# Optimization experiments

Hardware: AMD Instinct MI355X
Metric: run time of the kernel (lower is better)

## Reference

```python
import jax, jax.numpy as jnp
import numpy as np

B = 128
K = 16
# (in_ch, featdim, dim) per stage, matching conv1..conv11
DIMS = [(3, 8, 2048), (8, 32, 1024), (32, 64, 512), (64, 64, 256), (64, 64, 128),
        (64, 128, 64), (128, 256, 32), (256, 512, 16), (512, 512, 8), (512, 512, 4),
        (512, 1024, 2)]


def setup_inputs() -> dict:
    key = jax.random.key(0)
    ks = jax.random.split(key, 64)
    inp = {"x": jax.random.normal(ks[0], (B, 3, 2048), dtype=jnp.float32)}
    i = 1
    for li, (cin, cf, d) in enumerate(DIMS, start=1):
        inp[f"W{li}"] = jax.random.normal(ks[i], (3 * cf, cin), dtype=jnp.float32) / np.sqrt(cin).astype(np.float32); i += 1
        inp[f"b{li}"] = jax.random.normal(ks[i], (3 * cf,), dtype=jnp.float32) * 0.01; i += 1
        inp[f"sel{li}"] = jax.random.randint(ks[i], (d,), 0, 3); i += 1
    inp["fcW"] = jax.random.normal(ks[i], (K, 1024), dtype=jnp.float32) / np.sqrt(1024).astype(np.float32); i += 1
    inp["fcb"] = jax.random.normal(ks[i], (K,), dtype=jnp.float32) * 0.01
    return inp


def kdconv(x, W, b, sel, featdim, dim):
    # 1x1 conv == per-position matmul: x [B, Cin, dim] -> y [B, 3*featdim, dim]
    y = jax.nn.relu(jnp.einsum('oi,bin->bon', W, x) + b[None, :, None])
    y = y.reshape(-1, featdim, 3, dim)
    # kd split-dim gather: pick one of the 3 feature groups per position
    y = jnp.take_along_axis(y, sel[None, None, None, :], axis=2)[:, :, 0, :]  # [B, featdim, dim]
    # pairwise max-pool of sibling leaves
    return y.reshape(-1, featdim, dim // 2, 2).max(axis=-1)  # [B, featdim, dim//2]


def reference(x, sel1, sel2, sel3, sel4, sel5, sel6, sel7, sel8, sel9, sel10, sel11,
              W1, b1, W2, b2, W3, b3, W4, b4, W5, b5, W6, b6, W7, b7, W8, b8,
              W9, b9, W10, b10, W11, b11, fcW, fcb):
    Ws = [W1, W2, W3, W4, W5, W6, W7, W8, W9, W10, W11]
    bs = [b1, b2, b3, b4, b5, b6, b7, b8, b9, b10, b11]
    sels = [sel1, sel2, sel3, sel4, sel5, sel6, sel7, sel8, sel9, sel10, sel11]
    h = x
    for (cin, cf, d), W, b, s in zip(DIMS, Ws, bs, sels):
        h = kdconv(h, W, b, s, cf, d)
    h = h.reshape(-1, 1024)  # [B, 1024]
    return jax.nn.log_softmax(h @ fcW.T + fcb, axis=-1)
```

## Files before the change

kernel.cpp:

```cpp
#include <hip/hip_runtime.h>
#include <math.h>

typedef __attribute__((ext_vector_type(8))) short bf16x8;
typedef __attribute__((ext_vector_type(4))) float f32x4;

__device__ __forceinline__ unsigned short f2bf(float f) {
    unsigned u = __builtin_bit_cast(unsigned, f);
    u += 0x7FFF + ((u >> 16) & 1);
    return (unsigned short)(u >> 16);
}
__device__ __forceinline__ float bf2f(unsigned short h) {
    unsigned u = ((unsigned)h) << 16;
    return __builtin_bit_cast(float, u);
}

struct K1Params {
    const float* x;
    const float* W1; const float* B1; const int* S1;
    const float* W2; const float* B2; const int* S2;
    const float* Wsrc[6];
    unsigned short* Wb;
    unsigned short* X3;
};

__global__ __launch_bounds__(256) void k1_kernel(K1Params P)
{
    const int tid = threadIdx.x;

    if (blockIdx.x >= 128) {
        int gt = (blockIdx.x - 128) * 256 + tid;
        const int we[6] = {24576, 98304, 393216, 786432, 786432, 1572864};
        int off = 0;
#pragma unroll
        for (int li = 0; li < 6; ++li) {
            const float4* src = (const float4*)P.Wsrc[li];
            ushort4* dst = (ushort4*)(P.Wb + off);
            int n4 = we[li] >> 2;
            for (int i = gt; i < n4; i += 16384) {
                float4 w = src[i];
                dst[i] = make_ushort4(f2bf(w.x), f2bf(w.y), f2bf(w.z), f2bf(w.w));
            }
            off += we[li];
        }
        return;
    }

    __shared__ float wl1[72], bl1[24], wl2[768], bl2[96];
    __shared__ unsigned short bufL1[16 * 64 * 8];

    if (tid < 72) wl1[tid] = P.W1[tid];
    if (tid >= 128 && tid < 152) bl1[tid - 128] = P.B1[tid - 128];
    for (int i = tid; i < 768; i += 256) wl2[i] = P.W2[i];
    if (tid < 96) bl2[tid] = P.B2[tid];
    __syncthreads();

    const int npT = blockIdx.x >> 1;
    const int b0  = (blockIdx.x & 1) * 64;

    for (int i = tid; i < 1024; i += 256) {
        int pos_l = i >> 6, bl = i & 63;
        int np1 = npT * 16 + pos_l;
        int b = b0 + bl;
        int s0 = P.S1[2 * np1], s1 = P.S1[2 * np1 + 1];
        const float* xb = P.x + (size_t)b * 6144 + 2 * np1;
        float2 c0 = *(const float2*)(xb);
        float2 c1 = *(const float2*)(xb + 2048);
        float2 c2 = *(const float2*)(xb + 4096);
        unsigned short o[8];
#pragma unroll
        for (int f = 0; f < 8; ++f) {
            int r0 = f * 3 + s0, r1 = f * 3 + s1;
            float z0 = fmaf(wl1[r0*3+2], c2.x, fmaf(wl1[r0*3+1], c1.x, fmaf(wl1[r0*3+0], c0.x, bl1[r0])));
            float z1 = fmaf(wl1[r1*3+2], c2.y, fmaf(wl1[r1*3+1], c1.y, fmaf(wl1[r1*3+0], c0.y, bl1[r1])));
            o[f] = f2bf(fmaxf(fmaxf(z0, z1), 0.f));
        }
        unsigned short* dst = &bufL1[((size_t)pos_l * 64 + bl) * 8];
        *(ushort4*)dst       = make_ushort4(o[0], o[1], o[2], o[3]);
        *(ushort4*)(dst + 4) = make_ushort4(o[4], o[5], o[6], o[7]);
    }
    __syncthreads();

    for (int i = tid; i < 512; i += 256) {
        int np_l = i >> 6, bl = i & 63;
        int np2 = npT * 8 + np_l;
        int s0 = P.S2[2 * np2], s1 = P.S2[2 * np2 + 1];
        const unsigned short* r0 = &bufL1[((size_t)(2 * np_l) * 64 + bl) * 8];
        const unsigned short* r1 = &bufL1[((size_t)(2 * np_l + 1) * 64 + bl) * 8];
        float xa[8], xb[8];
        {
            ushort4 u0 = *(const ushort4*)r0, u1 = *(const ushort4*)(r0 + 4);
            ushort4 v0 = *(const ushort4*)r1, v1 = *(const ushort4*)(r1 + 4);
            xa[0]=bf2f(u0.x); xa[1]=bf2f(u0.y); xa[2]=bf2f(u0.z); xa[3]=bf2f(u0.w);
            xa[4]=bf2f(u1.x); xa[5]=bf2f(u1.y); xa[6]=bf2f(u1.z); xa[7]=bf2f(u1.w);
            xb[0]=bf2f(v0.x); xb[1]=bf2f(v0.y); xb[2]=bf2f(v0.z); xb[3]=bf2f(v0.w);
            xb[4]=bf2f(v1.x); xb[5]=bf2f(v1.y); xb[6]=bf2f(v1.z); xb[7]=bf2f(v1.w);
        }
        unsigned short o[32];
#pragma unroll
        for (int f = 0; f < 32; ++f) {
            const float* w0 = &wl2[(f * 3 + s0) * 8];
            const float* w1 = &wl2[(f * 3 + s1) * 8];
            float z0 = bl2[f * 3 + s0], z1 = bl2[f * 3 + s1];
#pragma unroll
            for (int k = 0; k < 8; ++k) {
                z0 = fmaf(w0[k], xa[k], z0);
                z1 = fmaf(w1[k], xb[k], z1);
            }
            o[f] = f2bf(fmaxf(fmaxf(z0, z1), 0.f));
        }
        unsigned short* dst = P.X3 + ((size_t)np2 * 128 + b0 + bl) * 32;
#pragma unroll
        for (int i2 = 0; i2 < 8; ++i2)
            *(ushort4*)(dst + 4 * i2) = make_ushort4(o[4*i2], o[4*i2+1], o[4*i2+2], o[4*i2+3]);
    }
}

template<int CIN>
__device__ __forceinline__ void mfma_tile(
    const unsigned short* a0, const unsigned short* a1,
    const unsigned short* b0p, const unsigned short* b1p,
    f32x4& acc0, f32x4& acc1)
{
#pragma unroll
    for (int k = 0; k < CIN; k += 32) {
        bf16x8 A0 = __builtin_bit_cast(bf16x8, *(const float4*)(const void*)(a0 + k));
        bf16x8 A1 = __builtin_bit_cast(bf16x8, *(const float4*)(const void*)(a1 + k));
        bf16x8 B0 = __builtin_bit_cast(bf16x8, *(const float4*)(const void*)(b0p + k));
        bf16x8 B1 = __builtin_bit_cast(bf16x8, *(const float4*)(const void*)(b1p + k));
        acc0 = __builtin_amdgcn_mfma_f32_16x16x32_bf16(A0, B0, acc0, 0, 0, 0);
        acc1 = __builtin_amdgcn_mfma_f32_16x16x32_bf16(A1, B1, acc1, 0, 0, 0);
    }
}

__device__ __forceinline__ void epilogue_store(
    unsigned short* dst, const f32x4& acc0, const f32x4& acc1,
    const float* bias, int fbase, int s0, int s1)
{
    unsigned short o[4];
#pragma unroll
    for (int r = 0; r < 4; ++r) {
        float v = fmaxf(fmaxf(acc0[r] + bias[(fbase + r) * 3 + s0],
                              acc1[r] + bias[(fbase + r) * 3 + s1]), 0.f);
        o[r] = f2bf(v);
    }
    *(ushort4*)dst = make_ushort4(o[0], o[1], o[2], o[3]);
}

__global__ __launch_bounds__(256) void stage2_kernel(
    const unsigned short* __restrict__ X3,
    const float* __restrict__ W3f, const float* __restrict__ B3, const int* __restrict__ S3,
    const float* __restrict__ W4f, const float* __restrict__ B4, const int* __restrict__ S4,
    const float* __restrict__ W5f, const float* __restrict__ B5, const int* __restrict__ S5,
    unsigned short* __restrict__ X6)
{
    __shared__ unsigned short W3l[6144];
    __shared__ unsigned short W4l[12288];
    __shared__ unsigned short W5l[12288];
    __shared__ unsigned short L3o[4 * 32 * 64];
    __shared__ unsigned short L4o[2 * 32 * 64];

    const int tid  = threadIdx.x;
    const int lane = tid & 63;
    const int wv   = tid >> 6;
    const int c = lane & 15, q = lane >> 4;
    const int n5 = blockIdx.x >> 2;
    const int b0 = (blockIdx.x & 3) * 32;

    for (int i = tid; i < 1536; i += 256) {
        float4 w = ((const float4*)W3f)[i];
        ((ushort4*)W3l)[i] = make_ushort4(f2bf(w.x), f2bf(w.y), f2bf(w.z), f2bf(w.w));
    }
    for (int i = tid; i < 3072; i += 256) {
        float4 w = ((const float4*)W4f)[i];
        ((ushort4*)W4l)[i] = make_ushort4(f2bf(w.x), f2bf(w.y), f2bf(w.z), f2bf(w.w));
        float4 v = ((const float4*)W5f)[i];
        ((ushort4*)W5l)[i] = make_ushort4(f2bf(v.x), f2bf(v.y), f2bf(v.z), f2bf(v.w));
    }
    __syncthreads();

    for (int t = wv; t < 32; t += 4) {
        int bt = t & 1, ft = (t >> 1) & 3, j = t >> 3;
        int np = 4 * n5 + j;
        int s0 = __builtin_amdgcn_readfirstlane(S3[2 * np]);
        int s1 = __builtin_amdgcn_readfirstlane(S3[2 * np + 1]);
        int f0 = ft * 16, bl = bt * 16;
        const unsigned short* a0 = &W3l[((f0 + c) * 3 + s0) * 32 + q * 8];
        const unsigned short* a1 = &W3l[((f0 + c) * 3 + s1) * 32 + q * 8];
        const unsigned short* bp0 = X3 + ((size_t)(8 * n5 + 2 * j) * 128 + b0 + bl + c) * 32 + q * 8;
        const unsigned short* bp1 = X3 + ((size_t)(8 * n5 + 2 * j + 1) * 128 + b0 + bl + c) * 32 + q * 8;
        f32x4 acc0 = {0.f,0.f,0.f,0.f}, acc1 = {0.f,0.f,0.f,0.f};
        mfma_tile<32>(a0, a1, bp0, bp1, acc0, acc1);
        epilogue_store(&L3o[((size_t)j * 32 + bl + c) * 64 + f0 + q * 4],
                       acc0, acc1, B3, f0 + q * 4, s0, s1);
    }
    __syncthreads();

    for (int t = wv; t < 16; t += 4) {
        int bt = t & 1, ft = (t >> 1) & 3, j = t >> 3;
        int np = 2 * n5 + j;
        int s0 = __builtin_amdgcn_readfirstlane(S4[2 * np]);
        int s1 = __builtin_amdgcn_readfirstlane(S4[2 * np + 1]);
        int f0 = ft * 16, bl = bt * 16;
        const unsigned short* a0 = &W4l[((f0 + c) * 3 + s0) * 64 + q * 8];
        const unsigned short* a1 = &W4l[((f0 + c) * 3 + s1) * 64 + q * 8];
        const unsigned short* bp0 = &L3o[((size_t)(2 * j) * 32 + bl + c) * 64 + q * 8];
        const unsigned short* bp1 = &L3o[((size_t)(2 * j + 1) * 32 + bl + c) * 64 + q * 8];
        f32x4 acc0 = {0.f,0.f,0.f,0.f}, acc1 = {0.f,0.f,0.f,0.f};
        mfma_tile<64>(a0, a1, bp0, bp1, acc0, acc1);
        epilogue_store(&L4o[((size_t)j * 32 + bl + c) * 64 + f0 + q * 4],
                       acc0, acc1, B4, f0 + q * 4, s0, s1);
    }
    __syncthreads();

    for (int t = wv; t < 8; t += 4) {
        int bt = t & 1, ft = t >> 1;
        int s0 = __builtin_amdgcn_readfirstlane(S5[2 * n5]);
        int s1 = __builtin_amdgcn_readfirstlane(S5[2 * n5 + 1]);
        int f0 = ft * 16, bl = bt * 16;
        const unsigned short* a0 = &W5l[((f0 + c) * 3 + s0) * 64 + q * 8];
        const unsigned short* a1 = &W5l[((f0 + c) * 3 + s1) * 64 + q * 8];
        const unsigned short* bp0 = &L4o[((size_t)(0) * 32 + bl + c) * 64 + q * 8];
        const unsigned short* bp1 = &L4o[((size_t)(1) * 32 + bl + c) * 64 + q * 8];
        f32x4 acc0 = {0.f,0.f,0.f,0.f}, acc1 = {0.f,0.f,0.f,0.f};
        mfma_tile<64>(a0, a1, bp0, bp1, acc0, acc1);
        epilogue_store(X6 + ((size_t)n5 * 128 + b0 + bl + c) * 64 + f0 + q * 4,
                       acc0, acc1, B5, f0 + q * 4, s0, s1);
    }
}

__global__ __launch_bounds__(512) void stage3_kernel(
    const unsigned short* __restrict__ X6,
    const unsigned short* __restrict__ W6b, const float* __restrict__ B6, const int* __restrict__ S6,
    const unsigned short* __restrict__ W7b, const float* __restrict__ B7, const int* __restrict__ S7,
    const unsigned short* __restrict__ W8b, const float* __restrict__ B8, const int* __restrict__ S8,
    unsigned short* __restrict__ X9)
{
    __shared__ unsigned short L6o[4 * 16 * 128];
    __shared__ unsigned short L7o[2 * 16 * 256];

    const int tid  = threadIdx.x;
    const int lane = tid & 63;
    const int wv   = tid >> 6;
    const int c = lane & 15, q = lane >> 4;
    const int n8 = blockIdx.x >> 3;
    const int b0 = (blockIdx.x & 7) * 16;

    for (int t = wv; t < 32; t += 8) {
        int ft = t & 7, j = t >> 3;
        int np = 4 * n8 + j;
        int s0 = __builtin_amdgcn_readfirstlane(S6[2 * np]);
        int s1 = __builtin_amdgcn_readfirstlane(S6[2 * np + 1]);
        int f0 = ft * 16;
        const unsigned short* a0 = W6b + (size_t)((f0 + c) * 3 + s0) * 64 + q * 8;
        const unsigned short* a1 = W6b + (size_t)((f0 + c) * 3 + s1) * 64 + q * 8;
        const unsigned short* bp0 = X6 + ((size_t)(8 * n8 + 2 * j) * 128 + b0 + c) * 64 + q * 8;
        const unsigned short* bp1 = X6 + ((size_t)(8 * n8 + 2 * j + 1) * 128 + b0 + c) * 64 + q * 8;
        f32x4 acc0 = {0.f,0.f,0.f,0.f}, acc1 = {0.f,0.f,0.f,0.f};
        mfma_tile<64>(a0, a1, bp0, bp1, acc0, acc1);
        epilogue_store(&L6o[((size_t)j * 16 + c) * 128 + f0 + q * 4],
                       acc0, acc1, B6, f0 + q * 4, s0, s1);
    }
    __syncthreads();

    for (int t = wv; t < 32; t += 8) {
        int ft = t & 15, j = t >> 4;
        int np = 2 * n8 + j;
        int s0 = __builtin_amdgcn_readfirstlane(S7[2 * np]);
        int s1 = __builtin_amdgcn_readfirstlane(S7[2 * np + 1]);
        int f0 = ft * 16;
        const unsigned short* a0 = W7b + (size_t)((f0 + c) * 3 + s0) * 128 + q * 8;
        const unsigned short* a1 = W7b + (size_t)((f0 + c) * 3 + s1) * 128 + q * 8;
        const unsigned short* bp0 = &L6o[((size_t)(2 * j) * 16 + c) * 128 + q * 8];
        const unsigned short* bp1 = &L6o[((size_t)(2 * j + 1) * 16 + c) * 128 + q * 8];
        f32x4 acc0 = {0.f,0.f,0.f,0.f}, acc1 = {0.f,0.f,0.f,0.f};
        mfma_tile<128>(a0, a1, bp0, bp1, acc0, acc1);
        epilogue_store(&L7o[((size_t)j * 16 + c) * 256 + f0 + q * 4],
                       acc0, acc1, B7, f0 + q * 4, s0, s1);
    }
    __syncthreads();

    {
        int s0 = __builtin_amdgcn_readfirstlane(S8[2 * n8]);
        int s1 = __builtin_amdgcn_readfirstlane(S8[2 * n8 + 1]);
        for (int t = wv; t < 32; t += 8) {
            int f0 = t * 16;
            const unsigned short* a0 = W8b + (size_t)((f0 + c) * 3 + s0) * 256 + q * 8;
            const unsigned short* a1 = W8b + (size_t)((f0 + c) * 3 + s1) * 256 + q * 8;
            const unsigned short* bp0 = &L7o[((size_t)(0) * 16 + c) * 256 + q * 8];
            const unsigned short* bp1 = &L7o[((size_t)(1) * 16 + c) * 256 + q * 8];
            f32x4 acc0 = {0.f,0.f,0.f,0.f}, acc1 = {0.f,0.f,0.f,0.f};
            mfma_tile<256>(a0, a1, bp0, bp1, acc0, acc1);
            epilogue_store(X9 + ((size_t)n8 * 128 + b0 + c) * 512 + f0 + q * 4,
                           acc0, acc1, B8, f0 + q * 4, s0, s1);
        }
    }
}

template<int CIN, int CF, int NP, int MW, int NW>
__global__ __launch_bounds__(256) void mfma_kernel(
    const unsigned short* __restrict__ Xin,
    const unsigned short* __restrict__ Wb,
    const float* __restrict__ bias,
    const int*   __restrict__ sel,
    unsigned short* __restrict__ Xout)
{
    constexpr int FT = CF / (16 * MW);
    constexpr int BT = 128 / (16 * NW);

    const int wid  = threadIdx.x >> 6;
    const int lane = threadIdx.x & 63;
    const int task = blockIdx.x * 4 + wid;
    const int bi = task % BT;
    const int fi = (task / BT) % FT;
    const int n  = task / (BT * FT);

    const int c = lane & 15;
    const int q = lane >> 4;
    const int s0 = __builtin_amdgcn_readfirstlane(sel[2 * n]);
    const int s1 = __builtin_amdgcn_readfirstlane(sel[2 * n + 1]);

    const int f0 = fi * 16 * MW;
    const int b0 = bi * 16 * NW;

    const unsigned short* ap[2][MW];
    const unsigned short* bp[2][NW];
#pragma unroll
    for (int p = 0; p < 2; ++p) {
        int s = p ? s1 : s0;
#pragma unroll
        for (int mi = 0; mi < MW; ++mi)
            ap[p][mi] = Wb + (size_t)((f0 + mi * 16 + c) * 3 + s) * CIN + q * 8;
#pragma unroll
        for (int ni = 0; ni < NW; ++ni)
            bp[p][ni] = Xin + ((size_t)(2 * n + p) * 128 + b0 + ni * 16 + c) * CIN + q * 8;
    }

    f32x4 acc[2][MW][NW];
#pragma unroll
    for (int p = 0; p < 2; ++p)
#pragma unroll
        for (int mi = 0; mi < MW; ++mi)
#pragma unroll
            for (int ni = 0; ni < NW; ++ni)
                acc[p][mi][ni] = (f32x4){0.f, 0.f, 0.f, 0.f};

#pragma unroll 2
    for (int k = 0; k < CIN; k += 32) {
        bf16x8 A[2][MW], B[2][NW];
#pragma unroll
        for (int p = 0; p < 2; ++p) {
#pragma unroll
            for (int mi = 0; mi < MW; ++mi)
                A[p][mi] = __builtin_bit_cast(bf16x8, *(const float4*)(const void*)(ap[p][mi] + k));
#pragma unroll
            for (int ni = 0; ni < NW; ++ni)
                B[p][ni] = __builtin_bit_cast(bf16x8, *(const float4*)(const void*)(bp[p][ni] + k));
        }
#pragma unroll
        for (int p = 0; p < 2; ++p)
#pragma unroll
            for (int mi = 0; mi < MW; ++mi)
#pragma unroll
                for (int ni = 0; ni < NW; ++ni)
                    acc[p][mi][ni] = __builtin_amdgcn_mfma_f32_16x16x32_bf16(
                        A[p][mi], B[p][ni], acc[p][mi][ni], 0, 0, 0);
    }

#pragma unroll
    for (int mi = 0; mi < MW; ++mi) {
        int fbase = f0 + mi * 16 + q * 4;
#pragma unroll
        for (int ni = 0; ni < NW; ++ni) {
            int b = b0 + ni * 16 + c;
            epilogue_store(Xout + ((size_t)n * 128 + b) * CF + fbase,
                           acc[0][mi][ni], acc[1][mi][ni], bias, fbase, s0, s1);
        }
    }
}

__global__ __launch_bounds__(256) void fc_logsoftmax_kernel(
    const unsigned short* __restrict__ h, const float* __restrict__ fcW,
    const float* __restrict__ fcb, float* __restrict__ out)
{
    int b   = blockIdx.x;
    int tid = threadIdx.x;
    int k     = tid & 15;
    int chunk = tid >> 4;

    const float* __restrict__ wk = fcW + (size_t)k * 1024;
    const unsigned short* hb = h + (size_t)b * 1024;

    float partial = 0.0f;
    int j0 = chunk * 64;
#pragma unroll 8
    for (int j = 0; j < 64; ++j)
        partial = fmaf(bf2f(hb[j0 + j]), wk[j0 + j], partial);

    __shared__ float red[16][17];
    red[chunk][k] = partial;
    __syncthreads();

    __shared__ float logits[16];
    if (tid < 16) {
        float s = fcb[tid];
#pragma unroll
        for (int c = 0; c < 16; ++c) s += red[c][tid];
        logits[tid] = s;
    }
    __syncthreads();

    if (tid < 16) {
        float mx = -INFINITY;
#pragma unroll
        for (int kk = 0; kk < 16; ++kk) mx = fmaxf(mx, logits[kk]);
        float se = 0.0f;
#pragma unroll
        for (int kk = 0; kk < 16; ++kk) se += expf(logits[kk] - mx);
        out[b * 16 + tid] = logits[tid] - mx - logf(se);
    }
}

extern "C" void kernel_launch(void* const* d_in, const int* in_sizes, int n_in,
                              void* d_out, int out_size, void* d_ws, size_t ws_size,
                              hipStream_t stream)
{
#define WL(i) (const float*)d_in[1 + 3 * (i)]
#define BL(i) (const float*)d_in[2 + 3 * (i)]
#define SL(i) (const int*)  d_in[3 + 3 * (i)]

    unsigned short* bufA = (unsigned short*)d_ws;
    unsigned short* bufB = bufA + 2u * 1024u * 1024u;
    unsigned short* Wb   = bufB + 2u * 1024u * 1024u;

    const int o6 = 0, o7 = 24576, o8 = 122880, o9 = 516096, o10 = 1302528, o11 = 2088960;

    K1Params P;
    P.x = (const float*)d_in[0];
    P.W1 = WL(0); P.B1 = BL(0); P.S1 = SL(0);
    P.W2 = WL(1); P.B2 = BL(1); P.S2 = SL(1);
    for (int i = 0; i < 6; ++i) P.Wsrc[i] = WL(5 + i);
    P.Wb = Wb; P.X3 = bufA;
    k1_kernel<<<192, 256, 0, stream>>>(P);

    stage2_kernel<<<256, 256, 0, stream>>>(bufA,
        WL(2), BL(2), SL(2), WL(3), BL(3), SL(3), WL(4), BL(4), SL(4), bufB);

    stage3_kernel<<<64, 512, 0, stream>>>(bufB,
        Wb + o6, BL(5), SL(5), Wb + o7, BL(6), SL(6), Wb + o8, BL(7), SL(7), bufA);

    mfma_kernel<512, 512, 4, 1, 2><<<128, 256, 0, stream>>>(bufA, Wb + o9,  BL(8),  SL(8),  bufB);
    mfma_kernel<512, 512, 2, 1, 2><<<64, 256, 0, stream>>>(bufB, Wb + o10, BL(9),  SL(9),  bufA);
    mfma_kernel<512, 1024, 1, 1, 2><<<64, 256, 0, stream>>>(bufA, Wb + o11, BL(10), SL(10), bufB);

    fc_logsoftmax_kernel<<<128, 256, 0, stream>>>(bufB, (const float*)d_in[34], (const float*)d_in[35], (float*)d_out);

#undef WL
#undef BL
#undef SL
}
```

Measured before the change: 237.4 us.

## Pre-convert stage-2 weights in k1 and split fused stage3 into per-layer MFMA kernels

The k1 kernel now also converts the W3-W5 weights to bf16, with twice as many conversion blocks. stage2 reads those bf16 weights from global memory instead of converting fp32 weights into LDS in every block. The LDS row stride for the intermediate tiles is padded to 72 to reduce bank conflicts. The fused stage3 kernel (64 blocks of 512 threads) is replaced by three launches of the generic mfma_kernel with more blocks. This trades one launch for three and loses the on-chip reuse of intermediates in exchange for more parallelism.

```diff
diff --git a/kernel.cpp b/kernel.cpp
--- a/kernel.cpp
+++ b/kernel.cpp
@@ -18,7 +18,7 @@
     const float* x;
     const float* W1; const float* B1; const int* S1;
     const float* W2; const float* B2; const int* S2;
-    const float* Wsrc[6];
+    const float* Wsrc[9];
     unsigned short* Wb;
     unsigned short* X3;
 };
@@ -29,14 +29,14 @@
 
     if (blockIdx.x >= 128) {
         int gt = (blockIdx.x - 128) * 256 + tid;
-        const int we[6] = {24576, 98304, 393216, 786432, 786432, 1572864};
+        const int we[9] = {6144, 12288, 12288, 24576, 98304, 393216, 786432, 786432, 1572864};
         int off = 0;
 #pragma unroll
-        for (int li = 0; li < 6; ++li) {
+        for (int li = 0; li < 9; ++li) {
             const float4* src = (const float4*)P.Wsrc[li];
             ushort4* dst = (ushort4*)(P.Wb + off);
             int n4 = we[li] >> 2;
-            for (int i = gt; i < n4; i += 16384) {
+            for (int i = gt; i < n4; i += 32768) {
                 float4 w = src[i];
                 dst[i] = make_ushort4(f2bf(w.x), f2bf(w.y), f2bf(w.z), f2bf(w.w));
             }
@@ -132,6 +132,23 @@
     }
 }
 
+template<int CIN, int RPE>
+__device__ __forceinline__ void mfma_tile_lds(
+    const unsigned short* a0, const unsigned short* a1,
+    const unsigned short* b0p, const unsigned short* b1p,
+    f32x4& acc0, f32x4& acc1)
+{
+#pragma unroll
+    for (int k = 0; k < CIN; k += 32) {
+        bf16x8 A0 = __builtin_bit_cast(bf16x8, *(const float4*)(const void*)(a0 + k));
+        bf16x8 A1 = __builtin_bit_cast(bf16x8, *(const float4*)(const void*)(a1 + k));
+        bf16x8 B0 = __builtin_bit_cast(bf16x8, *(const float4*)(const void*)(b0p + k));
+        bf16x8 B1 = __builtin_bit_cast(bf16x8, *(const float4*)(const void*)(b1p + k));
+        acc0 = __builtin_amdgcn_mfma_f32_16x16x32_bf16(A0, B0, acc0, 0, 0, 0);
+        acc1 = __builtin_amdgcn_mfma_f32_16x16x32_bf16(A1, B1, acc1, 0, 0, 0);
+    }
+}
+
 __device__ __forceinline__ void epilogue_store(
     unsigned short* dst, const f32x4& acc0, const f32x4& acc1,
     const float* bias, int fbase, int s0, int s1)
@@ -148,16 +165,15 @@
 
 __global__ __launch_bounds__(256) void stage2_kernel(
     const unsigned short* __restrict__ X3,
-    const float* __restrict__ W3f, const float* __restrict__ B3, const int* __restrict__ S3,
-    const float* __restrict__ W4f, const float* __restrict__ B4, const int* __restrict__ S4,
-    const float* __restrict__ W5f, const float* __restrict__ B5, const int* __restrict__ S5,
+    const unsigned short* __restrict__ Wb,
+    const float* __restrict__ B3, const int* __restrict__ S3,
+    const float* __restrict__ B4, const int* __restrict__ S4,
+    const float* __restrict__ B5, const int* __restrict__ S5,
     unsigned short* __restrict__ X6)
 {
-    __shared__ unsigned short W3l[6144];
-    __shared__ unsigned short W4l[12288];
-    __shared__ unsigned short W5l[12288];
-    __shared__ unsigned short L3o[4 * 32 * 64];
-    __shared__ unsigned short L4o[2 * 32 * 64];
+    constexpr int RPE = 72;
+    __shared__ unsigned short L3o[4 * 32 * RPE];
+    __shared__ unsigned short L4o[2 * 32 * RPE];
 
     const int tid  = threadIdx.x;
     const int lane = tid & 63;
@@ -166,17 +182,9 @@
     const int n5 = blockIdx.x >> 2;
     const int b0 = (blockIdx.x & 3) * 32;
 
-    for (int i = tid; i < 1536; i += 256) {
-        float4 w = ((const float4*)W3f)[i];
-        ((ushort4*)W3l)[i] = make_ushort4(f2bf(w.x), f2bf(w.y), f2bf(w.z), f2bf(w.w));
-    }
-    for (int i = tid; i < 3072; i += 256) {
-        float4 w = ((const float4*)W4f)[i];
-        ((ushort4*)W4l)[i] = make_ushort4(f2bf(w.x), f2bf(w.y), f2bf(w.z), f2bf(w.w));
-        float4 v = ((const float4*)W5f)[i];
-        ((ushort4*)W5l)[i] = make_ushort4(f2bf(v.x), f2bf(v.y), f2bf(v.z), f2bf(v.w));
-    }
-    __syncthreads();
+    const unsigned short* W3b = Wb;
+    const unsigned short* W4b = Wb + 6144;
+    const unsigned short* W5b = Wb + 18432;
 
     for (int t = wv; t < 32; t += 4) {
         int bt = t & 1, ft = (t >> 1) & 3, j = t >> 3;
@@ -184,13 +192,13 @@
         int s0 = __builtin_amdgcn_readfirstlane(S3[2 * np]);
         int s1 = __builtin_amdgcn_readfirstlane(S3[2 * np + 1]);
         int f0 = ft * 16, bl = bt * 16;
-        const unsigned short* a0 = &W3l[((f0 + c) * 3 + s0) * 32 + q * 8];
-        const unsigned short* a1 = &W3l[((f0 + c) * 3 + s1) * 32 + q * 8];
+        const unsigned short* a0 = W3b + (size_t)((f0 + c) * 3 + s0) * 32 + q * 8;
+        const unsigned short* a1 = W3b + (size_t)((f0 + c) * 3 + s1) * 32 + q * 8;
         const unsigned short* bp0 = X3 + ((size_t)(8 * n5 + 2 * j) * 128 + b0 + bl + c) * 32 + q * 8;
         const unsigned short* bp1 = X3 + ((size_t)(8 * n5 + 2 * j + 1) * 128 + b0 + bl + c) * 32 + q * 8;
         f32x4 acc0 = {0.f,0.f,0.f,0.f}, acc1 = {0.f,0.f,0.f,0.f};
         mfma_tile<32>(a0, a1, bp0, bp1, acc0, acc1);
-        epilogue_store(&L3o[((size_t)j * 32 + bl + c) * 64 + f0 + q * 4],
+        epilogue_store(&L3o[((size_t)j * 32 + bl + c) * RPE + f0 + q * 4],
                        acc0, acc1, B3, f0 + q * 4, s0, s1);
     }
     __syncthreads();
@@ -201,13 +209,13 @@
         int s0 = __builtin_amdgcn_readfirstlane(S4[2 * np]);
         int s1 = __builtin_amdgcn_readfirstlane(S4[2 * np + 1]);
         int f0 = ft * 16, bl = bt * 16;
-        const unsigned short* a0 = &W4l[((f0 + c) * 3 + s0) * 64 + q * 8];
-        const unsigned short* a1 = &W4l[((f0 + c) * 3 + s1) * 64 + q * 8];
-        const unsigned short* bp0 = &L3o[((size_t)(2 * j) * 32 + bl + c) * 64 + q * 8];
-        const unsigned short* bp1 = &L3o[((size_t)(2 * j + 1) * 32 + bl + c) * 64 + q * 8];
+        const unsigned short* a0 = W4b + (size_t)((f0 + c) * 3 + s0) * 64 + q * 8;
+        const unsigned short* a1 = W4b + (size_t)((f0 + c) * 3 + s1) * 64 + q * 8;
+        const unsigned short* bp0 = &L3o[((size_t)(2 * j) * 32 + bl + c) * RPE + q * 8];
+        const unsigned short* bp1 = &L3o[((size_t)(2 * j + 1) * 32 + bl + c) * RPE + q * 8];
         f32x4 acc0 = {0.f,0.f,0.f,0.f}, acc1 = {0.f,0.f,0.f,0.f};
-        mfma_tile<64>(a0, a1, bp0, bp1, acc0, acc1);
-        epilogue_store(&L4o[((size_t)j * 32 + bl + c) * 64 + f0 + q * 4],
+        mfma_tile_lds<64, RPE>(a0, a1, bp0, bp1, acc0, acc1);
+        epilogue_store(&L4o[((size_t)j * 32 + bl + c) * RPE + f0 + q * 4],
                        acc0, acc1, B4, f0 + q * 4, s0, s1);
     }
     __syncthreads();
@@ -217,82 +225,14 @@
         int s0 = __builtin_amdgcn_readfirstlane(S5[2 * n5]);
         int s1 = __builtin_amdgcn_readfirstlane(S5[2 * n5 + 1]);
         int f0 = ft * 16, bl = bt * 16;
-        const unsigned short* a0 = &W5l[((f0 + c) * 3 + s0) * 64 + q * 8];
-        const unsigned short* a1 = &W5l[((f0 + c) * 3 + s1) * 64 + q * 8];
-        const unsigned short* bp0 = &L4o[((size_t)(0) * 32 + bl + c) * 64 + q * 8];
-        const unsigned short* bp1 = &L4o[((size_t)(1) * 32 + bl + c) * 64 + q * 8];
+        const unsigned short* a0 = W5b + (size_t)((f0 + c) * 3 + s0) * 64 + q * 8;
+        const unsigned short* a1 = W5b + (size_t)((f0 + c) * 3 + s1) * 64 + q * 8;
+        const unsigned short* bp0 = &L4o[((size_t)(0) * 32 + bl + c) * RPE + q * 8];
+        const unsigned short* bp1 = &L4o[((size_t)(1) * 32 + bl + c) * RPE + q * 8];
         f32x4 acc0 = {0.f,0.f,0.f,0.f}, acc1 = {0.f,0.f,0.f,0.f};
-        mfma_tile<64>(a0, a1, bp0, bp1, acc0, acc1);
+        mfma_tile_lds<64, RPE>(a0, a1, bp0, bp1, acc0, acc1);
         epilogue_store(X6 + ((size_t)n5 * 128 + b0 + bl + c) * 64 + f0 + q * 4,
                        acc0, acc1, B5, f0 + q * 4, s0, s1);
-    }
-}
-
-__global__ __launch_bounds__(512) void stage3_kernel(
-    const unsigned short* __restrict__ X6,
-    const unsigned short* __restrict__ W6b, const float* __restrict__ B6, const int* __restrict__ S6,
-    const unsigned short* __restrict__ W7b, const float* __restrict__ B7, const int* __restrict__ S7,
-    const unsigned short* __restrict__ W8b, const float* __restrict__ B8, const int* __restrict__ S8,
-    unsigned short* __restrict__ X9)
-{
-    __shared__ unsigned short L6o[4 * 16 * 128];
-    __shared__ unsigned short L7o[2 * 16 * 256];
-
-    const int tid  = threadIdx.x;
-    const int lane = tid & 63;
-    const int wv   = tid >> 6;
-    const int c = lane & 15, q = lane >> 4;
-    const int n8 = blockIdx.x >> 3;
-    const int b0 = (blockIdx.x & 7) * 16;
-
-    for (int t = wv; t < 32; t += 8) {
-        int ft = t & 7, j = t >> 3;
-        int np = 4 * n8 + j;
-        int s0 = __builtin_amdgcn_readfirstlane(S6[2 * np]);
-        int s1 = __builtin_amdgcn_readfirstlane(S6[2 * np + 1]);
-        int f0 = ft * 16;
-        const unsigned short* a0 = W6b + (size_t)((f0 + c) * 3 + s0) * 64 + q * 8;
-        const unsigned short* a1 = W6b + (size_t)((f0 + c) * 3 + s1) * 64 + q * 8;
-        const unsigned short* bp0 = X6 + ((size_t)(8 * n8 + 2 * j) * 128 + b0 + c) * 64 + q * 8;
-        const unsigned short* bp1 = X6 + ((size_t)(8 * n8 + 2 * j + 1) * 128 + b0 + c) * 64 + q * 8;
-        f32x4 acc0 = {0.f,0.f,0.f,0.f}, acc1 = {0.f,0.f,0.f,0.f};
-        mfma_tile<64>(a0, a1, bp0, bp1, acc0, acc1);
-        epilogue_store(&L6o[((size_t)j * 16 + c) * 128 + f0 + q * 4],
-                       acc0, acc1, B6, f0 + q * 4, s0, s1);
-    }
-    __syncthreads();
-
-    for (int t = wv; t < 32; t += 8) {
-        int ft = t & 15, j = t >> 4;
-        int np = 2 * n8 + j;
-        int s0 = __builtin_amdgcn_readfirstlane(S7[2 * np]);
-        int s1 = __builtin_amdgcn_readfirstlane(S7[2 * np + 1]);
-        int f0 = ft * 16;
-        const unsigned short* a0 = W7b + (size_t)((f0 + c) * 3 + s0) * 128 + q * 8;
-        const unsigned short* a1 = W7b + (size_t)((f0 + c) * 3 + s1) * 128 + q * 8;
-        const unsigned short* bp0 = &L6o[((size_t)(2 * j) * 16 + c) * 128 + q * 8];
-        const unsigned short* bp1 = &L6o[((size_t)(2 * j + 1) * 16 + c) * 128 + q * 8];
-        f32x4 acc0 = {0.f,0.f,0.f,0.f}, acc1 = {0.f,0.f,0.f,0.f};
-        mfma_tile<128>(a0, a1, bp0, bp1, acc0, acc1);
-        epilogue_store(&L7o[((size_t)j * 16 + c) * 256 + f0 + q * 4],
-                       acc0, acc1, B7, f0 + q * 4, s0, s1);
-    }
-    __syncthreads();
-
-    {
-        int s0 = __builtin_amdgcn_readfirstlane(S8[2 * n8]);
-        int s1 = __builtin_amdgcn_readfirstlane(S8[2 * n8 + 1]);
-        for (int t = wv; t < 32; t += 8) {
-            int f0 = t * 16;
-            const unsigned short* a0 = W8b + (size_t)((f0 + c) * 3 + s0) * 256 + q * 8;
-            const unsigned short* a1 = W8b + (size_t)((f0 + c) * 3 + s1) * 256 + q * 8;
-            const unsigned short* bp0 = &L7o[((size_t)(0) * 16 + c) * 256 + q * 8];
-            const unsigned short* bp1 = &L7o[((size_t)(1) * 16 + c) * 256 + q * 8];
-            f32x4 acc0 = {0.f,0.f,0.f,0.f}, acc1 = {0.f,0.f,0.f,0.f};
-            mfma_tile<256>(a0, a1, bp0, bp1, acc0, acc1);
-            epilogue_store(X9 + ((size_t)n8 * 128 + b0 + c) * 512 + f0 + q * 4,
-                           acc0, acc1, B8, f0 + q * 4, s0, s1);
-        }
     }
 }
 
@@ -432,22 +372,24 @@
     unsigned short* bufB = bufA + 2u * 1024u * 1024u;
     unsigned short* Wb   = bufB + 2u * 1024u * 1024u;
 
-    const int o6 = 0, o7 = 24576, o8 = 122880, o9 = 516096, o10 = 1302528, o11 = 2088960;
+    const int o3 = 0, o4 = 6144, o5 = 18432, o6 = 30720, o7 = 55296,
+              o8 = 153600, o9 = 546816, o10 = 1333248, o11 = 2119680;
+    (void)o3; (void)o4; (void)o5;
 
     K1Params P;
     P.x = (const float*)d_in[0];
     P.W1 = WL(0); P.B1 = BL(0); P.S1 = SL(0);
     P.W2 = WL(1); P.B2 = BL(1); P.S2 = SL(1);
-    for (int i = 0; i < 6; ++i) P.Wsrc[i] = WL(5 + i);
+    for (int i = 0; i < 9; ++i) P.Wsrc[i] = WL(2 + i);
     P.Wb = Wb; P.X3 = bufA;
-    k1_kernel<<<192, 256, 0, stream>>>(P);
-
-    stage2_kernel<<<256, 256, 0, stream>>>(bufA,
-        WL(2), BL(2), SL(2), WL(3), BL(3), SL(3), WL(4), BL(4), SL(4), bufB);
-
-    stage3_kernel<<<64, 512, 0, stream>>>(bufB,
-        Wb + o6, BL(5), SL(5), Wb + o7, BL(6), SL(6), Wb + o8, BL(7), SL(7), bufA);
-
+    k1_kernel<<<256, 256, 0, stream>>>(P);
+
+    stage2_kernel<<<256, 256, 0, stream>>>(bufA, Wb,
+        BL(2), SL(2), BL(3), SL(3), BL(4), SL(4), bufB);
+
+    mfma_kernel<64, 128, 32, 2, 2><<<128, 256, 0, stream>>>(bufB, Wb + o6,  BL(5),  SL(5),  bufA);
+    mfma_kernel<128, 256, 16, 2, 2><<<128, 256, 0, stream>>>(bufA, Wb + o7,  BL(6),  SL(6),  bufB);
+    mfma_kernel<256, 512, 8, 2, 2><<<128, 256, 0, stream>>>(bufB, Wb + o8,  BL(7),  SL(7),  bufA);
     mfma_kernel<512, 512, 4, 1, 2><<<128, 256, 0, stream>>>(bufA, Wb + o9,  BL(8),  SL(8),  bufB);
     mfma_kernel<512, 512, 2, 1, 2><<<64, 256, 0, stream>>>(bufB, Wb + o10, BL(9),  SL(9),  bufA);
     mfma_kernel<512, 1024, 1, 1, 2><<<64, 256, 0, stream>>>(bufA, Wb + o11, BL(10), SL(10), bufB);
```

After: 217.8 us. 8.3% less time.
